# Optimization experiments

Hardware: AMD Instinct MI355X
Metric: run time of the kernel (lower is better)

The kernel has to match this reference:

```python
import jax, jax.numpy as jnp
import numpy as np

# Output shape from ToDenseMink.__init__:
#   batch=4, out_size=256, x = 512 // (2//1) = 256, y = 512 // (2//1) = 256
B, C, X, Y = 4, 256, 256, 256
N = 200000  # number of occupied sparse cells


def setup_inputs() -> dict:
    key = jax.random.key(0)
    kf, kc = jax.random.split(key)
    feats = jax.random.normal(kf, (N, C), dtype=jnp.float32)
    # Unique (batch, x, y) coordinates so the scatter is well-defined
    # (MinkowskiEngine sparse tensors have unique coordinates).
    lin = jax.random.permutation(kc, B * X * Y)[:N]
    b = lin // (X * Y)
    rem = lin % (X * Y)
    x = rem // Y
    y = rem % Y
    coords = jnp.stack([b, x, y], axis=-1).astype(jnp.int32)  # [N, 3]
    return {"feats": feats, "coords": coords}


def reference(feats, coords):
    # Equivalent of x.dense(shape=[B, C, X, Y], min_coordinate=0)[0]:
    # scatter each feature row into the dense grid at (batch, :, x, y).
    dense = jnp.zeros((B, C, X, Y), dtype=feats.dtype)
    dense = dense.at[coords[:, 0], :, coords[:, 1], coords[:, 2]].set(
        feats, mode="drop"
    )
    return dense
```

## Files before the change

### kernel.cpp

```cpp
#include <hip/hip_runtime.h>

#define BB 4
#define CC 256
#define XX 256
#define YY 256
#define NCELLS (BB * XX * YY)

__global__ void k_fill_idx(int4* __restrict__ idx4) {
    int i = blockIdx.x * blockDim.x + threadIdx.x;
    idx4[i] = make_int4(-1, -1, -1, -1);
}

__global__ void k_scatter_idx(const int* __restrict__ coords,
                              int* __restrict__ idx, int n) {
    int i = blockIdx.x * blockDim.x + threadIdx.x;
    if (i >= n) return;
    int b = coords[i * 3 + 0];
    int x = coords[i * 3 + 1];
    int y = coords[i * 3 + 2];
    if ((unsigned)b < BB && (unsigned)x < XX && (unsigned)y < YY) {
        idx[(b * XX + x) * YY + y] = i;
    }
}

__global__ void k_gather_out(const float4* __restrict__ feats4,
                             const int* __restrict__ idx,
                             float* __restrict__ out) {
    int bx = blockIdx.x;
    int y  = threadIdx.x;
    int b  = bx >> 8;
    int x  = bx & 255;

    int row = idx[bx * YY + y];
    bool valid = (row >= 0);
    const float4* fr = feats4 + (size_t)(valid ? row : 0) * (CC / 4);

    float* outp = out + ((size_t)b * CC * XX + x) * YY + y;

    #pragma unroll 4
    for (int c4 = 0; c4 < CC / 4; ++c4) {
        float4 v = fr[c4];
        if (!valid) { v.x = 0.f; v.y = 0.f; v.z = 0.f; v.w = 0.f; }
        int o = (c4 * 4) * (XX * YY);
        outp[o]               = v.x;
        outp[o + XX * YY]     = v.y;
        outp[o + 2 * XX * YY] = v.z;
        outp[o + 3 * XX * YY] = v.w;
    }
}

extern "C" void kernel_launch(void* const* d_in, const int* in_sizes, int n_in,
                              void* d_out, int out_size, void* d_ws, size_t ws_size,
                              hipStream_t stream) {
    const float* feats  = (const float*)d_in[0];
    const int*   coords = (const int*)d_in[1];
    int n = in_sizes[1] / 3;

    int*   idx   = (int*)d_ws;
    float* out   = (float*)d_out;

    k_fill_idx<<<NCELLS / 4 / 256, 256, 0, stream>>>((int4*)idx);

    k_scatter_idx<<<(n + 255) / 256, 256, 0, stream>>>(coords, idx, n);

    k_gather_out<<<BB * XX, 256, 0, stream>>>((const float4*)feats, idx, out);
}
```

Measured before the change: 406.7 us.

## Transpose gathered feature rows through swizzled LDS for coalesced reads and writes

Measured after the change: 414.3 us. About the same (+1.9%).

```diff
diff --git a/kernel.cpp b/kernel.cpp
--- a/kernel.cpp
+++ b/kernel.cpp
@@ -5,6 +5,9 @@
 #define XX 256
 #define YY 256
 #define NCELLS (BB * XX * YY)
+
+#define CH 32
+#define NCHUNK (CC / CH)
 
 __global__ void k_fill_idx(int4* __restrict__ idx4) {
     int i = blockIdx.x * blockDim.x + threadIdx.x;
@@ -23,29 +26,57 @@
     }
 }
 
-__global__ void k_gather_out(const float4* __restrict__ feats4,
-                             const int* __restrict__ idx,
-                             float* __restrict__ out) {
-    int bx = blockIdx.x;
-    int y  = threadIdx.x;
-    int b  = bx >> 8;
-    int x  = bx & 255;
+__global__ __launch_bounds__(256, 4) void k_gather_out(
+        const float4* __restrict__ feats4,
+        const int*    __restrict__ idx,
+        float*        __restrict__ out) {
+    __shared__ int   rowid[YY];
+    __shared__ float lds[CH][YY];
 
-    int row = idx[bx * YY + y];
-    bool valid = (row >= 0);
-    const float4* fr = feats4 + (size_t)(valid ? row : 0) * (CC / 4);
+    const int bx = blockIdx.x;
+    const int t  = threadIdx.x;
+    const int b  = bx >> 8;
+    const int x  = bx & 255;
 
-    float* outp = out + ((size_t)b * CC * XX + x) * YY + y;
+    rowid[t] = idx[bx * YY + t];
+    __syncthreads();
 
-    #pragma unroll 4
-    for (int c4 = 0; c4 < CC / 4; ++c4) {
-        float4 v = fr[c4];
-        if (!valid) { v.x = 0.f; v.y = 0.f; v.z = 0.f; v.w = 0.f; }
-        int o = (c4 * 4) * (XX * YY);
-        outp[o]               = v.x;
-        outp[o + XX * YY]     = v.y;
-        outp[o + 2 * XX * YY] = v.z;
-        outp[o + 3 * XX * YY] = v.w;
+    const int lane = t & 63;
+    const int w    = t >> 6;
+    const int sub  = lane & 7;
+    const int g    = lane >> 3;
+
+    const size_t out_base = ((size_t)b * CC * XX + x) * YY;
+
+    for (int ch = 0; ch < NCHUNK; ++ch) {
+        const int c0 = ch * CH;
+
+        #pragma unroll
+        for (int j = 0; j < 8; ++j) {
+            const int y = w * 64 + j * 8 + g;
+            const int r = rowid[y];
+            const bool valid = (r >= 0);
+            float4 v = feats4[(size_t)(valid ? r : 0) * (CC / 4)
+                              + (c0 >> 2) + sub];
+            if (!valid) { v.x = 0.f; v.y = 0.f; v.z = 0.f; v.w = 0.f; }
+            const int cl = sub * 4;
+            const int ys = y ^ (cl & 28);
+            lds[cl + 0][ys] = v.x;
+            lds[cl + 1][ys] = v.y;
+            lds[cl + 2][ys] = v.z;
+            lds[cl + 3][ys] = v.w;
+        }
+        __syncthreads();
+
+        #pragma unroll
+        for (int k = 0; k < 8; ++k) {
+            const int cl = w * 8 + k;
+            const int c  = c0 + cl;
+            const int ys = (lane * 4) ^ (cl & 28);
+            const float4 v = *(const float4*)&lds[cl][ys];
+            *(float4*)&out[out_base + (size_t)c * (XX * YY) + lane * 4] = v;
+        }
+        __syncthreads();
     }
 }
 
@@ -56,8 +87,8 @@
     const int*   coords = (const int*)d_in[1];
     int n = in_sizes[1] / 3;
 
-    int*   idx   = (int*)d_ws;
-    float* out   = (float*)d_out;
+    int*   idx = (int*)d_ws;
+    float* out = (float*)d_out;
 
     k_fill_idx<<<NCELLS / 4 / 256, 256, 0, stream>>>((int4*)idx);
 
```
